# Kernel optimization log

Hardware: AMD Instinct MI355X
Metric: run time of the kernel (lower is better)

Reference implementation:

```python
import jax, jax.numpy as jnp
import numpy as np
import math

B, H, S, D = 2, 16, 2048, 128

def setup_inputs() -> dict:
    key = jax.random.key(0)
    k1, k2, k3, k4 = jax.random.split(key, 4)
    x1 = jax.random.normal(k1, (B, H, S, D), dtype=jnp.float32)
    x2 = jax.random.normal(k2, (B, H, S, D), dtype=jnp.float32)
    x3 = jax.random.normal(k3, (B, H, D, S), dtype=jnp.float32)
    attn_mask = jax.random.normal(k4, (S, S), dtype=jnp.float32)
    return {"x1": x1, "x2": x2, "x3": x3, "attn_mask": attn_mask}

def reference(x1, x2, x3, attn_mask):
    scale = 1.0 / math.sqrt(x1.shape[-1])
    # [B,H,S,S] scores
    qk = jnp.einsum('bhqd,bhkd->bhqk', x1, x2) * scale + attn_mask
    attn_weight = jax.nn.softmax(qk, axis=-1)
    # x3 @ attn_weight : [B,H,D,S] @ [B,H,S,S] -> [B,H,D,S]
    output = jnp.einsum('bhds,bhsk->bhdk', x3, attn_weight)
    return output
```

## Files before the change

### kernel.cpp

```cpp
#include <hip/hip_runtime.h>


typedef __attribute__((ext_vector_type(8))) short short8;
typedef __attribute__((ext_vector_type(4))) float f32x4;

#define S_LEN 2048
#define D_LEN 128
#define BH_N 32
#define SCALE_QK 0.08838834764831845f

__device__ __forceinline__ unsigned short f2bf(float f) {
    union { float f; unsigned int i; } v; v.f = f;
    unsigned int r = v.i + 0x7FFFu + ((v.i >> 16) & 1u);
    return (unsigned short)(r >> 16);
}
__device__ __forceinline__ float bf2f(unsigned short u) {
    union { unsigned int i; float f; } v; v.i = ((unsigned int)u) << 16; return v.f;
}
__device__ __forceinline__ uint2 pack4bf(float4 v) {
    uint2 p;
    p.x = (unsigned)f2bf(v.x) | ((unsigned)f2bf(v.y) << 16);
    p.y = (unsigned)f2bf(v.z) | ((unsigned)f2bf(v.w) << 16);
    return p;
}

__global__ void k_cvt(const float* __restrict__ x1,
                      const float* __restrict__ x2,
                      const float* __restrict__ mask,
                      unsigned short* __restrict__ x1s,
                      unsigned short* __restrict__ x2b,
                      unsigned short* __restrict__ mbf) {
    const size_t N1 = (size_t)BH_N * S_LEN * D_LEN;
    const size_t NM = (size_t)S_LEN * S_LEN;
    size_t i = ((size_t)blockIdx.x * 256 + threadIdx.x) * 4;
    if (i < N1) {
        float4 v = *(const float4*)&x1[i];
        v.x *= SCALE_QK; v.y *= SCALE_QK; v.z *= SCALE_QK; v.w *= SCALE_QK;
        *(uint2*)&x1s[i] = pack4bf(v);
    } else if (i < 2 * N1) {
        size_t j = i - N1;
        float4 v = *(const float4*)&x2[j];
        *(uint2*)&x2b[j] = pack4bf(v);
    } else if (i < 2 * N1 + NM) {
        size_t j = i - 2 * N1;
        float4 v = *(const float4*)&mask[j];
        *(uint2*)&mbf[j] = pack4bf(v);
    }
}

__global__ __launch_bounds__(256, 2) void k_qk(
    const unsigned short* __restrict__ x1s,
    const unsigned short* __restrict__ x2b,
    const unsigned short* __restrict__ mbf,
    const float* __restrict__ x3,
    unsigned short* __restrict__ x3s)
{
    __shared__ unsigned short sQ[128 * 128];
    __shared__ unsigned short sK[128 * 128];
    __shared__ float sRSp[4][128];
    __shared__ float sRL[128];
    const int q0 = blockIdx.x * 128;
    const int bh = blockIdx.y;
    const unsigned short* x1p = x1s + (size_t)bh * S_LEN * D_LEN;
    const unsigned short* x2p = x2b + (size_t)bh * S_LEN * D_LEN;
    const int t = threadIdx.x;
    const int w = t >> 6, lane = t & 63, quad = lane >> 4, l16 = lane & 15;

#pragma unroll
    for (int i = 0; i < 8; ++i) {
        int idx = i * 256 + t;
        int r = idx >> 4, c = idx & 15;
        *(uint4*)&sQ[r * 128 + ((c ^ (r & 7)) * 8)] =
            *(const uint4*)&x1p[(size_t)(q0 + r) * D_LEN + c * 8];
    }

    float rs[8] = {0.f, 0.f, 0.f, 0.f, 0.f, 0.f, 0.f, 0.f};

    for (int k0 = 0; k0 < S_LEN; k0 += 128) {
        __syncthreads();
#pragma unroll
        for (int i = 0; i < 8; ++i) {
            int idx = i * 256 + t;
            int r = idx >> 4, c = idx & 15;
            *(uint4*)&sK[r * 128 + ((c ^ (r & 7)) * 8)] =
                *(const uint4*)&x2p[(size_t)(k0 + r) * D_LEN + c * 8];
        }
        __syncthreads();

        f32x4 acc[2][8];
#pragma unroll
        for (int kb = 0; kb < 2; ++kb)
#pragma unroll
            for (int qt = 0; qt < 8; ++qt) acc[kb][qt] = (f32x4){0.f, 0.f, 0.f, 0.f};
#pragma unroll
        for (int kk = 0; kk < 4; ++kk) {
            const int sc = ((kk * 4 + quad) ^ (l16 & 7)) * 8;
            short8 a[2];
#pragma unroll
            for (int kb = 0; kb < 2; ++kb)
                a[kb] = *(const short8*)&sK[(32 * w + kb * 16 + l16) * 128 + sc];
            short8 b[8];
#pragma unroll
            for (int qt = 0; qt < 8; ++qt)
                b[qt] = *(const short8*)&sQ[(qt * 16 + l16) * 128 + sc];
#pragma unroll
            for (int kb = 0; kb < 2; ++kb)
#pragma unroll
                for (int qt = 0; qt < 8; ++qt)
                    acc[kb][qt] = __builtin_amdgcn_mfma_f32_16x16x32_bf16(a[kb], b[qt], acc[kb][qt], 0, 0, 0);
        }
#pragma unroll
        for (int kb = 0; kb < 2; ++kb) {
            const int kg = k0 + 32 * w + 16 * kb + 4 * quad;
#pragma unroll
            for (int qt = 0; qt < 8; ++qt) {
                const int qg = q0 + qt * 16 + l16;
                uint2 m2 = *(const uint2*)&mbf[(size_t)qg * S_LEN + kg];
                float m0 = bf2f((unsigned short)(m2.x & 0xFFFF));
                float m1 = bf2f((unsigned short)(m2.x >> 16));
                float m2f = bf2f((unsigned short)(m2.y & 0xFFFF));
                float m3 = bf2f((unsigned short)(m2.y >> 16));
                rs[qt] += __expf(acc[kb][qt][0] + m0) + __expf(acc[kb][qt][1] + m1)
                        + __expf(acc[kb][qt][2] + m2f) + __expf(acc[kb][qt][3] + m3);
            }
        }
    }
#pragma unroll
    for (int qt = 0; qt < 8; ++qt) {
        float v = rs[qt];
        v += __shfl_xor(v, 16);
        v += __shfl_xor(v, 32);
        if (lane < 16) sRSp[w][qt * 16 + lane] = v;
    }
    __syncthreads();
    if (t < 128) {
        float tot = sRSp[0][t] + sRSp[1][t] + sRSp[2][t] + sRSp[3][t];
        sRL[t] = 1.0f / tot;
    }
    __syncthreads();

    const float* x3b = x3 + (size_t)bh * (size_t)D_LEN * S_LEN;
    unsigned short* x3sp = x3s + (size_t)bh * (size_t)D_LEN * S_LEN;
#pragma unroll
    for (int i = 0; i < 16; ++i) {
        int e = (i * 256 + t) * 4;
        int r = e >> 7, c = e & 127;
        float4 v = *(const float4*)&x3b[(size_t)r * S_LEN + q0 + c];
        v.x *= sRL[c]; v.y *= sRL[c + 1]; v.z *= sRL[c + 2]; v.w *= sRL[c + 3];
        *(uint2*)&x3sp[(size_t)r * S_LEN + q0 + c] = pack4bf(v);
    }
}

__global__ __launch_bounds__(256, 2) void k_out(
    const unsigned short* __restrict__ x1s,
    const unsigned short* __restrict__ x2b,
    const unsigned short* __restrict__ x3s,
    const unsigned short* __restrict__ mbf,
    float* __restrict__ out)
{
    __shared__ unsigned short sK[128 * 128];
    __shared__ unsigned short sQ[64 * 128];
    __shared__ unsigned short sX[128 * 64];
    __shared__ unsigned short sE[128 * 64];
    const int kb0 = blockIdx.x * 128;
    const int bh = blockIdx.y;
    const unsigned short* x1p = x1s + (size_t)bh * S_LEN * D_LEN;
    const unsigned short* x2p = x2b + (size_t)bh * S_LEN * D_LEN;
    const unsigned short* x3p = x3s + (size_t)bh * (size_t)D_LEN * S_LEN;
    const int t = threadIdx.x;
    const int w = t >> 6, lane = t & 63, quad = lane >> 4, l16 = lane & 15;

#pragma unroll
    for (int i = 0; i < 8; ++i) {
        int idx = i * 256 + t;
        int r = idx >> 4, c = idx & 15;
        *(uint4*)&sK[r * 128 + ((c ^ (r & 7)) * 8)] =
            *(const uint4*)&x2p[(size_t)(kb0 + r) * D_LEN + c * 8];
    }

    f32x4 oa[16];
#pragma unroll
    for (int i = 0; i < 16; ++i) oa[i] = (f32x4){0.f, 0.f, 0.f, 0.f};

    for (int q0 = 0; q0 < S_LEN; q0 += 64) {
        __syncthreads();
#pragma unroll
        for (int i = 0; i < 4; ++i) {
            int idx = i * 256 + t;
            int r = idx >> 4, c = idx & 15;
            *(uint4*)&sQ[r * 128 + ((c ^ (r & 7)) * 8)] =
                *(const uint4*)&x1p[(size_t)(q0 + r) * D_LEN + c * 8];
        }
#pragma unroll
        for (int i = 0; i < 4; ++i) {
            int idx = i * 256 + t;
            int r = idx >> 3, c = idx & 7;
            *(uint4*)&sX[r * 64 + ((c ^ (r & 7)) * 8)] =
                *(const uint4*)&x3p[(size_t)r * S_LEN + q0 + c * 8];
        }
        __syncthreads();

        f32x4 acc[8];
#pragma unroll
        for (int kb = 0; kb < 8; ++kb) acc[kb] = (f32x4){0.f, 0.f, 0.f, 0.f};
#pragma unroll
        for (int kk = 0; kk < 4; ++kk) {
            const int sc = ((kk * 4 + quad) ^ (l16 & 7)) * 8;
            short8 a = *(const short8*)&sQ[(16 * w + l16) * 128 + sc];
            short8 b[8];
#pragma unroll
            for (int kb = 0; kb < 8; ++kb)
                b[kb] = *(const short8*)&sK[(kb * 16 + l16) * 128 + sc];
#pragma unroll
            for (int kb = 0; kb < 8; ++kb)
                acc[kb] = __builtin_amdgcn_mfma_f32_16x16x32_bf16(a, b[kb], acc[kb], 0, 0, 0);
        }
        const int qrow = 16 * w + 4 * quad;
        const int qoff7 = (16 * w + 4 * quad) & 7;
        const int cE = (16 * w + 4 * quad) >> 3;
#pragma unroll
        for (int kb = 0; kb < 8; ++kb) {
            const int kg = kb0 + kb * 16 + l16;
            unsigned short e4[4];
#pragma unroll
            for (int r = 0; r < 4; ++r) {
                float m = bf2f(mbf[(size_t)(q0 + qrow + r) * S_LEN + kg]);
                e4[r] = f2bf(__expf(acc[kb][r] + m));
            }
            uint2 pk;
            pk.x = (unsigned)e4[0] | ((unsigned)e4[1] << 16);
            pk.y = (unsigned)e4[2] | ((unsigned)e4[3] << 16);
            const int krow = kb * 16 + l16;
            *(uint2*)&sE[krow * 64 + ((cE ^ (krow & 7)) * 8) + qoff7] = pk;
        }
        __syncthreads();

#pragma unroll
        for (int kk = 0; kk < 2; ++kk) {
            const int sc = ((kk * 4 + quad) ^ (l16 & 7)) * 8;
            short8 a[2];
#pragma unroll
            for (int db = 0; db < 2; ++db)
                a[db] = *(const short8*)&sX[(32 * w + 16 * db + l16) * 64 + sc];
            short8 b[8];
#pragma unroll
            for (int kb = 0; kb < 8; ++kb)
                b[kb] = *(const short8*)&sE[(kb * 16 + l16) * 64 + sc];
#pragma unroll
            for (int db = 0; db < 2; ++db)
#pragma unroll
                for (int kb = 0; kb < 8; ++kb)
                    oa[db * 8 + kb] = __builtin_amdgcn_mfma_f32_16x16x32_bf16(a[db], b[kb], oa[db * 8 + kb], 0, 0, 0);
        }
    }

#pragma unroll
    for (int db = 0; db < 2; ++db)
#pragma unroll
        for (int kb = 0; kb < 8; ++kb)
#pragma unroll
            for (int r = 0; r < 4; ++r) {
                int d = 32 * w + 16 * db + 4 * quad + r;
                out[((size_t)bh * D_LEN + d) * S_LEN + kb0 + kb * 16 + l16] =
                    oa[db * 8 + kb][r];
            }
}

__global__ __launch_bounds__(256, 3) void k_rowsum_fb(
    const float* __restrict__ x1, const float* __restrict__ x2,
    const float* __restrict__ mask, float* __restrict__ rl)
{
    __shared__ unsigned short sQ[128 * 136];
    __shared__ unsigned short sK[64 * 136];
    const int q0 = blockIdx.x * 128;
    const int bh = blockIdx.y;
    const float* x1b = x1 + (size_t)bh * S_LEN * D_LEN;
    const float* x2b = x2 + (size_t)bh * S_LEN * D_LEN;
    const int t = threadIdx.x;
    const int w = t >> 6, lane = t & 63, quad = lane >> 4, l16 = lane & 15;
#pragma unroll
    for (int i = 0; i < 16; ++i) {
        int e = (i * 256 + t) * 4;
        int r = e >> 7, c = e & 127;
        float4 v = *(const float4*)&x1b[(size_t)(q0 + r) * D_LEN + c];
        *(uint2*)&sQ[r * 136 + c] = pack4bf(v);
    }
    float rs[8] = {0.f, 0.f, 0.f, 0.f, 0.f, 0.f, 0.f, 0.f};
    for (int k0 = 0; k0 < S_LEN; k0 += 64) {
        __syncthreads();
#pragma unroll
        for (int i = 0; i < 8; ++i) {
            int e = (i * 256 + t) * 4;
            int r = e >> 7, c = e & 127;
            float4 v = *(const float4*)&x2b[(size_t)(k0 + r) * D_LEN + c];
            *(uint2*)&sK[r * 136 + c] = pack4bf(v);
        }
        __syncthreads();
#pragma unroll
        for (int qb = 0; qb < 2; ++qb) {
            const int qrow = 32 * w + 16 * qb;
#pragma unroll
            for (int kb = 0; kb < 4; ++kb) {
                f32x4 acc = {0.f, 0.f, 0.f, 0.f};
#pragma unroll
                for (int kk = 0; kk < 4; ++kk) {
                    short8 a = *(const short8*)&sQ[(qrow + l16) * 136 + kk * 32 + quad * 8];
                    short8 b = *(const short8*)&sK[(kb * 16 + l16) * 136 + kk * 32 + quad * 8];
                    acc = __builtin_amdgcn_mfma_f32_16x16x32_bf16(a, b, acc, 0, 0, 0);
                }
                const int kg = k0 + kb * 16 + l16;
                const int qg = q0 + qrow + 4 * quad;
#pragma unroll
                for (int r = 0; r < 4; ++r) {
                    float m = mask[(size_t)(qg + r) * S_LEN + kg];
                    rs[qb * 4 + r] += __expf(acc[r] * SCALE_QK + m);
                }
            }
        }
    }
#pragma unroll
    for (int i = 0; i < 8; ++i) {
        float v = rs[i];
        v += __shfl_xor(v, 1); v += __shfl_xor(v, 2);
        v += __shfl_xor(v, 4); v += __shfl_xor(v, 8);
        if (l16 == 0) {
            int qg = q0 + 32 * w + 16 * (i >> 2) + 4 * quad + (i & 3);
            rl[(size_t)bh * S_LEN + qg] = 1.0f / v;
        }
    }
}

__global__ __launch_bounds__(256, 2) void k_out_fb(
    const float* __restrict__ x1, const float* __restrict__ x2,
    const float* __restrict__ x3, const float* __restrict__ mask,
    const float* __restrict__ rl, float* __restrict__ out)
{
    __shared__ unsigned short sK[64 * 136];
    __shared__ unsigned short sQ[64 * 136];
    __shared__ unsigned short sX[128 * 72];
    __shared__ unsigned short sE[64 * 72];
    const int kb0 = blockIdx.x * 64;
    const int bh = blockIdx.y;
    const float* x1b = x1 + (size_t)bh * S_LEN * D_LEN;
    const float* x2b = x2 + (size_t)bh * S_LEN * D_LEN;
    const float* x3b = x3 + (size_t)bh * (size_t)D_LEN * S_LEN;
    const float* rlb = rl + (size_t)bh * S_LEN;
    const int t = threadIdx.x;
    const int w = t >> 6, lane = t & 63, quad = lane >> 4, l16 = lane & 15;
#pragma unroll
    for (int i = 0; i < 8; ++i) {
        int e = (i * 256 + t) * 4;
        int r = e >> 7, c = e & 127;
        float4 v = *(const float4*)&x2b[(size_t)(kb0 + r) * D_LEN + c];
        *(uint2*)&sK[r * 136 + c] = pack4bf(v);
    }
    f32x4 oa[8];
#pragma unroll
    for (int i = 0; i < 8; ++i) oa[i] = (f32x4){0.f, 0.f, 0.f, 0.f};
    for (int q0 = 0; q0 < S_LEN; q0 += 64) {
        __syncthreads();
#pragma unroll
        for (int i = 0; i < 8; ++i) {
            int e = (i * 256 + t) * 4;
            int r = e >> 7, c = e & 127;
            float4 v = *(const float4*)&x1b[(size_t)(q0 + r) * D_LEN + c];
            *(uint2*)&sQ[r * 136 + c] = pack4bf(v);
        }
#pragma unroll
        for (int i = 0; i < 8; ++i) {
            int e = (i * 256 + t) * 4;
            int r = e >> 6, c = e & 63;
            float4 v = *(const float4*)&x3b[(size_t)r * S_LEN + q0 + c];
            *(uint2*)&sX[r * 72 + c] = pack4bf(v);
        }
        __syncthreads();
        const int qrow = 16 * w + 4 * quad;
        float rl4[4];
#pragma unroll
        for (int r = 0; r < 4; ++r) rl4[r] = rlb[q0 + qrow + r];
#pragma unroll
        for (int kb = 0; kb < 4; ++kb) {
            f32x4 acc = {0.f, 0.f, 0.f, 0.f};
#pragma unroll
            for (int kk = 0; kk < 4; ++kk) {
                short8 a = *(const short8*)&sQ[(16 * w + l16) * 136 + kk * 32 + quad * 8];
                short8 b = *(const short8*)&sK[(kb * 16 + l16) * 136 + kk * 32 + quad * 8];
                acc = __builtin_amdgcn_mfma_f32_16x16x32_bf16(a, b, acc, 0, 0, 0);
            }
            const int kg = kb0 + kb * 16 + l16;
            unsigned short e4[4];
#pragma unroll
            for (int r = 0; r < 4; ++r) {
                float m = mask[(size_t)(q0 + qrow + r) * S_LEN + kg];
                e4[r] = f2bf(__expf(acc[r] * SCALE_QK + m) * rl4[r]);
            }
            uint2 pk;
            pk.x = (unsigned)e4[0] | ((unsigned)e4[1] << 16);
            pk.y = (unsigned)e4[2] | ((unsigned)e4[3] << 16);
            *(uint2*)&sE[(kb * 16 + l16) * 72 + qrow] = pk;
        }
        __syncthreads();
#pragma unroll
        for (int db = 0; db < 2; ++db)
#pragma unroll
            for (int kb = 0; kb < 4; ++kb) {
                f32x4 a0 = oa[db * 4 + kb];
#pragma unroll
                for (int kk = 0; kk < 2; ++kk) {
                    short8 a = *(const short8*)&sX[(32 * w + 16 * db + l16) * 72 + kk * 32 + quad * 8];
                    short8 b = *(const short8*)&sE[(kb * 16 + l16) * 72 + kk * 32 + quad * 8];
                    a0 = __builtin_amdgcn_mfma_f32_16x16x32_bf16(a, b, a0, 0, 0, 0);
                }
                oa[db * 4 + kb] = a0;
            }
    }
#pragma unroll
    for (int db = 0; db < 2; ++db)
#pragma unroll
        for (int kb = 0; kb < 4; ++kb)
#pragma unroll
            for (int r = 0; r < 4; ++r) {
                int d = 32 * w + 16 * db + 4 * quad + r;
                out[((size_t)bh * D_LEN + d) * S_LEN + kb0 + kb * 16 + l16] =
                    oa[db * 4 + kb][r];
            }
}

extern "C" void kernel_launch(void* const* d_in, const int* in_sizes, int n_in,
                              void* d_out, int out_size, void* d_ws, size_t ws_size,
                              hipStream_t stream) {
    const float* x1 = (const float*)d_in[0];
    const float* x2 = (const float*)d_in[1];
    const float* x3 = (const float*)d_in[2];
    const float* mask = (const float*)d_in[3];
    float* out = (float*)d_out;

    const size_t N1 = (size_t)BH_N * S_LEN * D_LEN;
    const size_t NM = (size_t)S_LEN * S_LEN;
    const size_t need = (3 * N1 + NM) * sizeof(unsigned short);

    if (ws_size >= need) {
        unsigned short* x1s = (unsigned short*)d_ws;
        unsigned short* x2b = x1s + N1;
        unsigned short* x3s = x2b + N1;
        unsigned short* mbf = x3s + N1;
        const size_t tot4 = (2 * N1 + NM) / 4;
        k_cvt<<<dim3((unsigned)(tot4 / 256)), dim3(256), 0, stream>>>(x1, x2, mask, x1s, x2b, mbf);
        k_qk<<<dim3(S_LEN / 128, BH_N), dim3(256), 0, stream>>>(x1s, x2b, mbf, x3, x3s);
        k_out<<<dim3(S_LEN / 128, BH_N), dim3(256), 0, stream>>>(x1s, x2b, x3s, mbf, out);
    } else {
        float* rl = (float*)d_ws;
        k_rowsum_fb<<<dim3(S_LEN / 128, BH_N), dim3(256), 0, stream>>>(x1, x2, mask, rl);
        k_out_fb<<<dim3(S_LEN / 64, BH_N), dim3(256), 0, stream>>>(x1, x2, x3, mask, rl, out);
    }
}
```

Baseline: 336.6 us.

## Fold log2e into inputs, use exp2, prefetch mask, swap QK operand roles

Pre-multiplies the Q scale and the mask by log2(e) during conversion so both kernels can use exp2f directly instead of __expf. Mask values are prefetched into registers before the MFMA loop, and s_setprio raises wave priority around the MFMA blocks. The QK kernel swaps operands so each wave owns query rows, which turns the row-sum reduction into intra-lane shuffles and removes the shared partial-sum buffer. exp results are packed to bf16 with the hardware v_cvt_pk_bf16_f32 instruction, at the cost of more live registers for the prefetched mask and uncoalesced 2-byte mask loads.

```diff
diff --git a/kernel.cpp b/kernel.cpp
--- a/kernel.cpp
+++ b/kernel.cpp
@@ -8,6 +8,7 @@
 #define D_LEN 128
 #define BH_N 32
 #define SCALE_QK 0.08838834764831845f
+#define LOG2E 1.4426950408889634f
 
 __device__ __forceinline__ unsigned short f2bf(float f) {
     union { float f; unsigned int i; } v; v.f = f;
@@ -22,6 +23,11 @@
     p.x = (unsigned)f2bf(v.x) | ((unsigned)f2bf(v.y) << 16);
     p.y = (unsigned)f2bf(v.z) | ((unsigned)f2bf(v.w) << 16);
     return p;
+}
+__device__ __forceinline__ unsigned cvt_pk_bf16(float lo, float hi) {
+    unsigned r;
+    asm("v_cvt_pk_bf16_f32 %0, %1, %2" : "=v"(r) : "v"(lo), "v"(hi));
+    return r;
 }
 
 __global__ void k_cvt(const float* __restrict__ x1,
@@ -33,9 +39,10 @@
     const size_t N1 = (size_t)BH_N * S_LEN * D_LEN;
     const size_t NM = (size_t)S_LEN * S_LEN;
     size_t i = ((size_t)blockIdx.x * 256 + threadIdx.x) * 4;
+    const float s1 = SCALE_QK * LOG2E;
     if (i < N1) {
         float4 v = *(const float4*)&x1[i];
-        v.x *= SCALE_QK; v.y *= SCALE_QK; v.z *= SCALE_QK; v.w *= SCALE_QK;
+        v.x *= s1; v.y *= s1; v.z *= s1; v.w *= s1;
         *(uint2*)&x1s[i] = pack4bf(v);
     } else if (i < 2 * N1) {
         size_t j = i - N1;
@@ -44,6 +51,7 @@
     } else if (i < 2 * N1 + NM) {
         size_t j = i - 2 * N1;
         float4 v = *(const float4*)&mask[j];
+        v.x *= LOG2E; v.y *= LOG2E; v.z *= LOG2E; v.w *= LOG2E;
         *(uint2*)&mbf[j] = pack4bf(v);
     }
 }
@@ -57,7 +65,6 @@
 {
     __shared__ unsigned short sQ[128 * 128];
     __shared__ unsigned short sK[128 * 128];
-    __shared__ float sRSp[4][128];
     __shared__ float sRL[128];
     const int q0 = blockIdx.x * 128;
     const int bh = blockIdx.y;
@@ -87,55 +94,58 @@
         }
         __syncthreads();
 
+        unsigned short mpf[2][8][4];
+#pragma unroll
+        for (int qb = 0; qb < 2; ++qb)
+#pragma unroll
+            for (int kb = 0; kb < 8; ++kb)
+#pragma unroll
+                for (int rr = 0; rr < 4; ++rr)
+                    mpf[qb][kb][rr] =
+                        mbf[(size_t)(q0 + 32 * w + 16 * qb + 4 * quad + rr) * S_LEN
+                            + k0 + kb * 16 + l16];
+
         f32x4 acc[2][8];
 #pragma unroll
-        for (int kb = 0; kb < 2; ++kb)
-#pragma unroll
-            for (int qt = 0; qt < 8; ++qt) acc[kb][qt] = (f32x4){0.f, 0.f, 0.f, 0.f};
+        for (int qb = 0; qb < 2; ++qb)
+#pragma unroll
+            for (int kb = 0; kb < 8; ++kb) acc[qb][kb] = (f32x4){0.f, 0.f, 0.f, 0.f};
+
+        __builtin_amdgcn_s_setprio(1);
 #pragma unroll
         for (int kk = 0; kk < 4; ++kk) {
             const int sc = ((kk * 4 + quad) ^ (l16 & 7)) * 8;
             short8 a[2];
 #pragma unroll
-            for (int kb = 0; kb < 2; ++kb)
-                a[kb] = *(const short8*)&sK[(32 * w + kb * 16 + l16) * 128 + sc];
+            for (int qb = 0; qb < 2; ++qb)
+                a[qb] = *(const short8*)&sQ[(32 * w + 16 * qb + l16) * 128 + sc];
             short8 b[8];
 #pragma unroll
-            for (int qt = 0; qt < 8; ++qt)
-                b[qt] = *(const short8*)&sQ[(qt * 16 + l16) * 128 + sc];
-#pragma unroll
-            for (int kb = 0; kb < 2; ++kb)
-#pragma unroll
-                for (int qt = 0; qt < 8; ++qt)
-                    acc[kb][qt] = __builtin_amdgcn_mfma_f32_16x16x32_bf16(a[kb], b[qt], acc[kb][qt], 0, 0, 0);
-        }
-#pragma unroll
-        for (int kb = 0; kb < 2; ++kb) {
-            const int kg = k0 + 32 * w + 16 * kb + 4 * quad;
-#pragma unroll
-            for (int qt = 0; qt < 8; ++qt) {
-                const int qg = q0 + qt * 16 + l16;
-                uint2 m2 = *(const uint2*)&mbf[(size_t)qg * S_LEN + kg];
-                float m0 = bf2f((unsigned short)(m2.x & 0xFFFF));
-                float m1 = bf2f((unsigned short)(m2.x >> 16));
-                float m2f = bf2f((unsigned short)(m2.y & 0xFFFF));
-                float m3 = bf2f((unsigned short)(m2.y >> 16));
-                rs[qt] += __expf(acc[kb][qt][0] + m0) + __expf(acc[kb][qt][1] + m1)
-                        + __expf(acc[kb][qt][2] + m2f) + __expf(acc[kb][qt][3] + m3);
-            }
-        }
-    }
-#pragma unroll
-    for (int qt = 0; qt < 8; ++qt) {
-        float v = rs[qt];
-        v += __shfl_xor(v, 16);
-        v += __shfl_xor(v, 32);
-        if (lane < 16) sRSp[w][qt * 16 + lane] = v;
-    }
-    __syncthreads();
-    if (t < 128) {
-        float tot = sRSp[0][t] + sRSp[1][t] + sRSp[2][t] + sRSp[3][t];
-        sRL[t] = 1.0f / tot;
+            for (int kb = 0; kb < 8; ++kb)
+                b[kb] = *(const short8*)&sK[(kb * 16 + l16) * 128 + sc];
+#pragma unroll
+            for (int qb = 0; qb < 2; ++qb)
+#pragma unroll
+                for (int kb = 0; kb < 8; ++kb)
+                    acc[qb][kb] = __builtin_amdgcn_mfma_f32_16x16x32_bf16(a[qb], b[kb], acc[qb][kb], 0, 0, 0);
+        }
+        __builtin_amdgcn_s_setprio(0);
+
+#pragma unroll
+        for (int qb = 0; qb < 2; ++qb)
+#pragma unroll
+            for (int kb = 0; kb < 8; ++kb)
+#pragma unroll
+                for (int rr = 0; rr < 4; ++rr)
+                    rs[qb * 4 + rr] += exp2f(acc[qb][kb][rr] + bf2f(mpf[qb][kb][rr]));
+    }
+
+#pragma unroll
+    for (int i = 0; i < 8; ++i) {
+        float v = rs[i];
+        v += __shfl_xor(v, 1); v += __shfl_xor(v, 2);
+        v += __shfl_xor(v, 4); v += __shfl_xor(v, 8);
+        if (l16 == 0) sRL[32 * w + 16 * (i >> 2) + 4 * quad + (i & 3)] = 1.0f / v;
     }
     __syncthreads();
 
@@ -169,6 +179,9 @@
     const unsigned short* x3p = x3s + (size_t)bh * (size_t)D_LEN * S_LEN;
     const int t = threadIdx.x;
     const int w = t >> 6, lane = t & 63, quad = lane >> 4, l16 = lane & 15;
+    const int qrow = 16 * w + 4 * quad;
+    const int cE = qrow >> 3;
+    const int qoff7 = qrow & 7;
 
 #pragma unroll
     for (int i = 0; i < 8; ++i) {
@@ -200,9 +213,17 @@
         }
         __syncthreads();
 
+        unsigned short mpf[8][4];
+#pragma unroll
+        for (int kb = 0; kb < 8; ++kb)
+#pragma unroll
+            for (int rr = 0; rr < 4; ++rr)
+                mpf[kb][rr] = mbf[(size_t)(q0 + qrow + rr) * S_LEN + kb0 + kb * 16 + l16];
+
         f32x4 acc[8];
 #pragma unroll
         for (int kb = 0; kb < 8; ++kb) acc[kb] = (f32x4){0.f, 0.f, 0.f, 0.f};
+        __builtin_amdgcn_s_setprio(1);
 #pragma unroll
         for (int kk = 0; kk < 4; ++kk) {
             const int sc = ((kk * 4 + quad) ^ (l16 & 7)) * 8;
@@ -215,26 +236,23 @@
             for (int kb = 0; kb < 8; ++kb)
                 acc[kb] = __builtin_amdgcn_mfma_f32_16x16x32_bf16(a, b[kb], acc[kb], 0, 0, 0);
         }
-        const int qrow = 16 * w + 4 * quad;
-        const int qoff7 = (16 * w + 4 * quad) & 7;
-        const int cE = (16 * w + 4 * quad) >> 3;
+        __builtin_amdgcn_s_setprio(0);
+
 #pragma unroll
         for (int kb = 0; kb < 8; ++kb) {
-            const int kg = kb0 + kb * 16 + l16;
-            unsigned short e4[4];
-#pragma unroll
-            for (int r = 0; r < 4; ++r) {
-                float m = bf2f(mbf[(size_t)(q0 + qrow + r) * S_LEN + kg]);
-                e4[r] = f2bf(__expf(acc[kb][r] + m));
-            }
+            float e0 = exp2f(acc[kb][0] + bf2f(mpf[kb][0]));
+            float e1 = exp2f(acc[kb][1] + bf2f(mpf[kb][1]));
+            float e2 = exp2f(acc[kb][2] + bf2f(mpf[kb][2]));
+            float e3 = exp2f(acc[kb][3] + bf2f(mpf[kb][3]));
             uint2 pk;
-            pk.x = (unsigned)e4[0] | ((unsigned)e4[1] << 16);
-            pk.y = (unsigned)e4[2] | ((unsigned)e4[3] << 16);
+            pk.x = cvt_pk_bf16(e0, e1);
+            pk.y = cvt_pk_bf16(e2, e3);
             const int krow = kb * 16 + l16;
             *(uint2*)&sE[krow * 64 + ((cE ^ (krow & 7)) * 8) + qoff7] = pk;
         }
         __syncthreads();
 
+        __builtin_amdgcn_s_setprio(1);
 #pragma unroll
         for (int kk = 0; kk < 2; ++kk) {
             const int sc = ((kk * 4 + quad) ^ (l16 & 7)) * 8;
@@ -252,6 +270,7 @@
                 for (int kb = 0; kb < 8; ++kb)
                     oa[db * 8 + kb] = __builtin_amdgcn_mfma_f32_16x16x32_bf16(a[db], b[kb], oa[db * 8 + kb], 0, 0, 0);
         }
+        __builtin_amdgcn_s_setprio(0);
     }
 
 #pragma unroll
@@ -259,10 +278,10 @@
 #pragma unroll
         for (int kb = 0; kb < 8; ++kb)
 #pragma unroll
-            for (int r = 0; r < 4; ++r) {
-                int d = 32 * w + 16 * db + 4 * quad + r;
+            for (int rr = 0; rr < 4; ++rr) {
+                int d = 32 * w + 16 * db + 4 * quad + rr;
                 out[((size_t)bh * D_LEN + d) * S_LEN + kb0 + kb * 16 + l16] =
-                    oa[db * 8 + kb][r];
+                    oa[db * 8 + kb][rr];
             }
 }
 
```

Measured after the change: 310.6 us. -7.7%, faster.
